# Optimization experiments

Measured on AMD Instinct MI355X. Metric: run time of the kernel, lower is better.

The kernel has to match this reference:

```python
import jax, jax.numpy as jnp
import numpy as np

TEMP = 0.5
EPS = 1e-8  # torch CosineSimilarity eps


def setup_inputs() -> dict:
    key = jax.random.key(0)
    k1, k2 = jax.random.split(key)
    B, D = 4096, 512
    z_i = jax.random.normal(k1, (B, D), dtype=jnp.float32)
    z_j = jax.random.normal(k2, (B, D), dtype=jnp.float32)
    return {"z_i": z_i, "z_j": z_j}


def reference(z_i, z_j):
    B = z_i.shape[0]
    N = 2 * B
    z = jnp.concatenate([z_i, z_j], axis=0)              # [N, D]
    norm = jnp.maximum(jnp.linalg.norm(z, axis=1, keepdims=True), EPS)
    zn = z / norm                                        # unit rows
    sim = jnp.matmul(zn, zn.T) / TEMP                    # [N, N] cosine sims / temperature
    # positives: sim[i, i+B] for i<B and sim[i+B, i] for i<B
    pos = jnp.concatenate([jnp.diagonal(sim, offset=B), jnp.diagonal(sim, offset=-B)])  # [N]
    # CE over logits [pos, negatives] with label 0 == -pos + logsumexp(row without diagonal)
    diag_mask = jnp.eye(N, dtype=bool)
    sim_masked = jnp.where(diag_mask, -jnp.inf, sim)
    lse = jax.nn.logsumexp(sim_masked, axis=1)           # [N]
    loss = jnp.sum(lse - pos) / N                        # CrossEntropyLoss(reduction='sum') / N
    return loss
```

## Files before the change

kernel.cpp:

```cpp
#include <hip/hip_runtime.h>
#include <stdint.h>

#define NROWS 8192
#define HALF_N 4096
#define DIM 512
#define INV_TEMP 2.0f
#define E2SCALE 2.8853900817779268f
#define LN2 0.6931471805599453f
#define NTILES 1056
#define NXCD 8
#define TPX (NTILES / NXCD)

typedef int i32x8 __attribute__((ext_vector_type(8)));
typedef float f32x16 __attribute__((ext_vector_type(16)));

__device__ __forceinline__ void gload_lds16(const unsigned char* g, unsigned char* l) {
  __builtin_amdgcn_global_load_lds(
      (const __attribute__((address_space(1))) unsigned int*)(uintptr_t)g,
      (__attribute__((address_space(3))) unsigned int*)(uint32_t)(uintptr_t)l,
      16, 0, 0);
}

__global__ void __launch_bounds__(256) k_normalize(const float* __restrict__ zi,
                                                   const float* __restrict__ zj,
                                                   unsigned char* __restrict__ zn,
                                                   float* __restrict__ sumexp) {
  int tid = threadIdx.x;
  int gid = blockIdx.x * 256 + tid;
  if (gid < NROWS) sumexp[gid] = 0.0f;
  int wave = tid >> 6, lane = tid & 63;
  int row = blockIdx.x * 4 + wave;
  const float* src = (row < HALF_N) ? (zi + (size_t)row * DIM)
                                    : (zj + (size_t)(row - HALF_N) * DIM);
  const float4* s4 = (const float4*)src;
  float4 a = s4[lane];
  float4 b = s4[lane + 64];
  float ss = a.x * a.x + a.y * a.y + a.z * a.z + a.w * a.w +
             b.x * b.x + b.y * b.y + b.z * b.z + b.w * b.w;
#pragma unroll
  for (int off = 32; off > 0; off >>= 1) ss += __shfl_xor(ss, off, 64);
  float inv = 1.0f / fmaxf(sqrtf(ss), 1e-8f);
  int w0 = __builtin_amdgcn_cvt_pk_fp8_f32(a.x * inv, a.y * inv, 0, false);
  w0 = __builtin_amdgcn_cvt_pk_fp8_f32(a.z * inv, a.w * inv, w0, true);
  int w1 = __builtin_amdgcn_cvt_pk_fp8_f32(b.x * inv, b.y * inv, 0, false);
  w1 = __builtin_amdgcn_cvt_pk_fp8_f32(b.z * inv, b.w * inv, w1, true);
  unsigned char* dst = zn + (size_t)row * DIM;
  *((int*)(dst + lane * 4)) = w0;
  *((int*)(dst + 256 + lane * 4)) = w1;
}

__global__ void __launch_bounds__(256, 2) k_simsum(const unsigned char* __restrict__ zn,
                                                   float* __restrict__ sumexp,
                                                   float* __restrict__ posv) {
  __shared__ __align__(16) unsigned char As[3][256 * 64];
  __shared__ __align__(16) unsigned char Bs[3][128 * 64];
  int tid = threadIdx.x;
  int wave = tid >> 6, lane = tid & 63;

  int b = blockIdx.x;
  int idx = (b & (NXCD - 1)) * TPX + (b >> 3);
  int tm = (int)((65.0f - sqrtf(4225.0f - 4.0f * idx)) * 0.5f);
  while (tm * (65 - tm) > idx) tm--;
  while ((tm + 1) * (64 - tm) <= idx) tm++;
  int tn = idx - tm * (63 - tm);
  int rowBase = tm * 256, colBase = tn * 128;

  int wr = (wave >> 1) * 128, wc = (wave & 1) * 64;
  int h = lane >> 5, c32 = lane & 31;

  int rA = wave * 64 + (lane >> 2);
  int cA = (lane & 3) ^ ((rA >> 1) & 3);
  const unsigned char* gA = zn + (size_t)(rowBase + rA) * DIM + cA * 16;
  int rB = wave * 32 + (lane >> 2);
  int cB = (lane & 3) ^ ((rB >> 1) & 3);
  const unsigned char* gB = zn + (size_t)(colBase + rB) * DIM + cB * 16;

#define STAGE(bf)                                     \
  do {                                                \
    unsigned char* la = &As[bf][wave * 4096];         \
    unsigned char* lb = &Bs[bf][wave * 2048];         \
    gload_lds16(gA, la);                              \
    gload_lds16(gA + 16 * DIM, la + 1024);            \
    gload_lds16(gA + 32 * DIM, la + 2048);            \
    gload_lds16(gA + 48 * DIM, la + 3072);            \
    gload_lds16(gB, lb);                              \
    gload_lds16(gB + 16 * DIM, lb + 1024);            \
    gA += 64; gB += 64;                               \
  } while (0)

  f32x16 acc[4][2];
#pragma unroll
  for (int i = 0; i < 4; i++)
#pragma unroll
    for (int j = 0; j < 2; j++)
#pragma unroll
      for (int r = 0; r < 16; r++) acc[i][j][r] = 0.f;

  int sg = (c32 >> 1) & 3;
  int p0 = (2 * h) ^ sg, p1 = p0 ^ 1;
  int aIdx[4] = {(wr + c32) * 4, (wr + 32 + c32) * 4,
                 (wr + 64 + c32) * 4, (wr + 96 + c32) * 4};
  int bIdx[2] = {(wc + c32) * 4, (wc + 32 + c32) * 4};

#define COMPUTE(bf)                                                                  \
  do {                                                                               \
    const int4* Av = (const int4*)As[bf];                                            \
    const int4* Bv = (const int4*)Bs[bf];                                            \
    i32x8 af[4], bfr[2];                                                             \
    _Pragma("unroll") for (int i = 0; i < 4; i++) {                                  \
      int4 lo = Av[aIdx[i] + p0], hi = Av[aIdx[i] + p1];                             \
      af[i] = (i32x8){lo.x, lo.y, lo.z, lo.w, hi.x, hi.y, hi.z, hi.w};               \
    }                                                                                \
    _Pragma("unroll") for (int j = 0; j < 2; j++) {                                  \
      int4 lo = Bv[bIdx[j] + p0], hi = Bv[bIdx[j] + p1];                             \
      bfr[j] = (i32x8){lo.x, lo.y, lo.z, lo.w, hi.x, hi.y, hi.z, hi.w};              \
    }                                                                                \
    __builtin_amdgcn_s_setprio(1);                                                   \
    _Pragma("unroll") for (int i = 0; i < 4; i++)                                    \
      _Pragma("unroll") for (int j = 0; j < 2; j++)                                  \
        acc[i][j] = __builtin_amdgcn_mfma_scale_f32_32x32x64_f8f6f4(                 \
            af[i], bfr[j], acc[i][j], 0, 0,                               \
            0, 0x7F, 0, 0x7F);                                     \
    __builtin_amdgcn_s_setprio(0);                                                   \
  } while (0)

#define ASM_VMCNT(n) asm volatile("s_waitcnt vmcnt(" #n ")" ::: "memory")
#define WINDOW(s, vm)                                        \
  do {                                                       \
    ASM_VMCNT(vm);                                           \
    asm volatile("s_waitcnt lgkmcnt(0)" ::: "memory");       \
    __builtin_amdgcn_sched_barrier(0);                       \
    __builtin_amdgcn_s_barrier();                            \
    __builtin_amdgcn_sched_barrier(0);                       \
    if ((s) + 2 < 8) STAGE(((s) + 2) % 3);                   \
    COMPUTE((s) % 3);                                        \
  } while (0)

  STAGE(0);
  STAGE(1);
  WINDOW(0, 6);
  WINDOW(1, 6);
  WINDOW(2, 6);
  WINDOW(3, 6);
  WINDOW(4, 6);
  WINDOW(5, 6);
  WINDOW(6, 6);
  WINDOW(7, 0);

  int dbase = colBase + wc - rowBase - wr;
  int rsel = (c32 & 3) | ((c32 >> 3) << 2);
  bool diagLane = (h == ((c32 >> 2) & 1));

#pragma unroll
  for (int i = 0; i < 4; i++)
#pragma unroll
    for (int j = 0; j < 2; j++) {
      int d = dbase + j * 32 - i * 32;
      if (d == HALF_N && diagLane) {
        float sv = acc[i][j][rsel] * INV_TEMP;
        int gr = rowBase + wr + i * 32 + c32;
        posv[gr] = sv;
        posv[gr + HALF_N] = sv;
      }
    }

  float cp[2] = {0.f, 0.f};
#pragma unroll
  for (int i = 0; i < 4; i++) {
    int d0 = dbase - i * 32;
    int d1 = d0 + 32;
#pragma unroll
    for (int r = 0; r < 16; r++) {
      int rowIn = (r & 3) + 8 * (r >> 2) + 4 * h;
      float e0 = __builtin_amdgcn_exp2f(acc[i][0][r] * E2SCALE);
      float e1 = __builtin_amdgcn_exp2f(acc[i][1][r] * E2SCALE);
      bool k0 = (d0 > 0) || ((d0 == 0) && (rowIn < c32));
      bool k1 = (d1 > 0) || ((d1 == 0) && (rowIn < c32));
      e0 = k0 ? e0 : 0.f;
      e1 = k1 ? e1 : 0.f;
      cp[0] += e0;
      cp[1] += e1;
      acc[i][0][r] = e0 + e1;
    }
  }

#define FOLD5(RPX)                                                 \
  do {                                                             \
    _Pragma("unroll") for (int t = 0; t < 16; t++) {               \
      float mine = (lane & 16) ? RPX(t + 16) : RPX(t);             \
      float oth = __shfl_xor((lane & 16) ? RPX(t) : RPX(t + 16), 16, 64); \
      RPX(t) = mine + oth;                                         \
    }                                                              \
    _Pragma("unroll") for (int t = 0; t < 8; t++) {                \
      float mine = (lane & 8) ? RPX(t + 8) : RPX(t);               \
      float oth = __shfl_xor((lane & 8) ? RPX(t) : RPX(t + 8), 8, 64); \
      RPX(t) = mine + oth;                                         \
    }                                                              \
    _Pragma("unroll") for (int t = 0; t < 4; t++) {                \
      float mine = (lane & 4) ? RPX(t + 4) : RPX(t);               \
      float oth = __shfl_xor((lane & 4) ? RPX(t) : RPX(t + 4), 4, 64); \
      RPX(t) = mine + oth;                                         \
    }                                                              \
    _Pragma("unroll") for (int t = 0; t < 2; t++) {                \
      float mine = (lane & 2) ? RPX(t + 2) : RPX(t);               \
      float oth = __shfl_xor((lane & 2) ? RPX(t) : RPX(t + 2), 2, 64); \
      RPX(t) = mine + oth;                                         \
    }                                                              \
    {                                                              \
      float mine = (lane & 1) ? RPX(1) : RPX(0);                   \
      float oth = __shfl_xor((lane & 1) ? RPX(0) : RPX(1), 1, 64); \
      RPX(0) = mine + oth;                                         \
    }                                                              \
  } while (0)

#define RPA(t) acc[(t) >> 4][0][(t) & 15]
#define RPB(t) acc[2 + ((t) >> 4)][0][(t) & 15]
  int myrow = rowBase + wr + 32 * (c32 >> 4) + (c32 & 3) + 8 * ((c32 >> 2) & 3) + 4 * h;
  FOLD5(RPA);
  atomicAdd(&sumexp[myrow], RPA(0));
  FOLD5(RPB);
  atomicAdd(&sumexp[myrow + 64], RPB(0));
#undef RPA
#undef RPB

  cp[0] += __shfl_xor(cp[0], 32, 64);
  cp[1] += __shfl_xor(cp[1], 32, 64);
  float cv = h ? cp[1] : cp[0];
  atomicAdd(&sumexp[colBase + wc + h * 32 + c32], cv);
#undef STAGE
#undef COMPUTE
#undef WINDOW
#undef ASM_VMCNT
#undef FOLD5
}

__global__ void __launch_bounds__(1024) k_final(const float* __restrict__ sumexp,
                                                const float* __restrict__ posv,
                                                float* __restrict__ out) {
  __shared__ float red[16];
  int tid = threadIdx.x;
  const float4* se4 = (const float4*)sumexp;
  const float4* pv4 = (const float4*)posv;
  float p = 0.f;
#pragma unroll
  for (int c = 0; c < 2; c++) {
    float4 se = se4[tid * 2 + c];
    float4 pv = pv4[tid * 2 + c];
    p += (__builtin_amdgcn_logf(se.x) + __builtin_amdgcn_logf(se.y) +
          __builtin_amdgcn_logf(se.z) + __builtin_amdgcn_logf(se.w)) * LN2 -
         (pv.x + pv.y + pv.z + pv.w);
  }
#pragma unroll
  for (int off = 32; off > 0; off >>= 1) p += __shfl_xor(p, off, 64);
  int wv = tid >> 6, ln = tid & 63;
  if (ln == 0) red[wv] = p;
  __syncthreads();
  if (tid == 0) {
    float t = 0.f;
    for (int w = 0; w < 16; w++) t += red[w];
    out[0] = t / (float)NROWS;
  }
}

extern "C" void kernel_launch(void* const* d_in, const int* in_sizes, int n_in,
                              void* d_out, int out_size, void* d_ws, size_t ws_size,
                              hipStream_t stream) {
  const float* zi = (const float*)d_in[0];
  const float* zj = (const float*)d_in[1];
  unsigned char* zn = (unsigned char*)d_ws;
  float* sumexp = (float*)((char*)d_ws + (size_t)NROWS * DIM);
  float* posv = sumexp + NROWS;
  float* out = (float*)d_out;

  hipLaunchKernelGGL(k_normalize, dim3(2048), dim3(256), 0, stream, zi, zj, zn, sumexp);
  hipLaunchKernelGGL(k_simsum, dim3(NTILES), dim3(256), 0, stream, zn, sumexp, posv);
  hipLaunchKernelGGL(k_final, dim3(1), dim3(1024), 0, stream, sumexp, posv, out);
}
```

Measured before the change: 97.15 us.

## Load MFMA operands directly from global memory into registers, dropping LDS staging

Replaces the triple-buffered LDS pipeline (global_load_lds plus barriers) with per-wave direct global loads of the fp8 operand fragments into registers, double-buffered across K steps. This removes LDS traffic, s_barrier synchronisation and LDS occupancy limits. In exchange, operand rows shared between waves are now fetched redundantly from global/L2, and many more VGPRs are needed for the two register buffers, which may hurt occupancy or latency hiding.

```diff
diff --git a/kernel.cpp b/kernel.cpp
--- a/kernel.cpp
+++ b/kernel.cpp
@@ -13,13 +13,6 @@
 
 typedef int i32x8 __attribute__((ext_vector_type(8)));
 typedef float f32x16 __attribute__((ext_vector_type(16)));
-
-__device__ __forceinline__ void gload_lds16(const unsigned char* g, unsigned char* l) {
-  __builtin_amdgcn_global_load_lds(
-      (const __attribute__((address_space(1))) unsigned int*)(uintptr_t)g,
-      (__attribute__((address_space(3))) unsigned int*)(uint32_t)(uintptr_t)l,
-      16, 0, 0);
-}
 
 __global__ void __launch_bounds__(256) k_normalize(const float* __restrict__ zi,
                                                    const float* __restrict__ zj,
@@ -52,8 +45,6 @@
 __global__ void __launch_bounds__(256, 2) k_simsum(const unsigned char* __restrict__ zn,
                                                    float* __restrict__ sumexp,
                                                    float* __restrict__ posv) {
-  __shared__ __align__(16) unsigned char As[3][256 * 64];
-  __shared__ __align__(16) unsigned char Bs[3][128 * 64];
   int tid = threadIdx.x;
   int wave = tid >> 6, lane = tid & 63;
 
@@ -68,84 +59,78 @@
   int wr = (wave >> 1) * 128, wc = (wave & 1) * 64;
   int h = lane >> 5, c32 = lane & 31;
 
-  int rA = wave * 64 + (lane >> 2);
-  int cA = (lane & 3) ^ ((rA >> 1) & 3);
-  const unsigned char* gA = zn + (size_t)(rowBase + rA) * DIM + cA * 16;
-  int rB = wave * 32 + (lane >> 2);
-  int cB = (lane & 3) ^ ((rB >> 1) & 3);
-  const unsigned char* gB = zn + (size_t)(colBase + rB) * DIM + cB * 16;
-
-#define STAGE(bf)                                     \
-  do {                                                \
-    unsigned char* la = &As[bf][wave * 4096];         \
-    unsigned char* lb = &Bs[bf][wave * 2048];         \
-    gload_lds16(gA, la);                              \
-    gload_lds16(gA + 16 * DIM, la + 1024);            \
-    gload_lds16(gA + 32 * DIM, la + 2048);            \
-    gload_lds16(gA + 48 * DIM, la + 3072);            \
-    gload_lds16(gB, lb);                              \
-    gload_lds16(gB + 16 * DIM, lb + 1024);            \
-    gA += 64; gB += 64;                               \
+  const unsigned char* pA0 = zn + (size_t)(rowBase + wr + c32) * DIM + h * 32;
+  const unsigned char* pA1 = pA0 + 32 * DIM;
+  const unsigned char* pA2 = pA0 + 64 * DIM;
+  const unsigned char* pA3 = pA0 + 96 * DIM;
+  const unsigned char* pB0 = zn + (size_t)(colBase + wc + c32) * DIM + h * 32;
+  const unsigned char* pB1 = pB0 + 32 * DIM;
+
+  f32x16 acc[4][2];
+#pragma unroll
+  for (int i = 0; i < 4; i++)
+#pragma unroll
+    for (int j = 0; j < 2; j++)
+#pragma unroll
+      for (int r = 0; r < 16; r++) acc[i][j][r] = 0.f;
+
+#define PACK8(lo, hi) ((i32x8){lo.x, lo.y, lo.z, lo.w, hi.x, hi.y, hi.z, hi.w})
+#define MF(a, b, c)                                                       \
+  __builtin_amdgcn_mfma_scale_f32_32x32x64_f8f6f4((a), (b), (c), 0, 0,    \
+                                                  0, 0x7F, 0, 0x7F)
+
+  int4 Xa0l, Xa0h, Xa1l, Xa1h, Xa2l, Xa2h, Xa3l, Xa3h, Xb0l, Xb0h, Xb1l, Xb1h;
+  int4 Ya0l, Ya0h, Ya1l, Ya1h, Ya2l, Ya2h, Ya3l, Ya3h, Yb0l, Yb0h, Yb1l, Yb1h;
+
+#define LOADSET(P, koff)                                                  \
+  do {                                                                    \
+    P##a0l = *(const int4*)(pA0 + (koff));                                \
+    P##a0h = *(const int4*)(pA0 + (koff) + 16);                           \
+    P##a1l = *(const int4*)(pA1 + (koff));                                \
+    P##a1h = *(const int4*)(pA1 + (koff) + 16);                           \
+    P##a2l = *(const int4*)(pA2 + (koff));                                \
+    P##a2h = *(const int4*)(pA2 + (koff) + 16);                           \
+    P##a3l = *(const int4*)(pA3 + (koff));                                \
+    P##a3h = *(const int4*)(pA3 + (koff) + 16);                           \
+    P##b0l = *(const int4*)(pB0 + (koff));                                \
+    P##b0h = *(const int4*)(pB0 + (koff) + 16);                           \
+    P##b1l = *(const int4*)(pB1 + (koff));                                \
+    P##b1h = *(const int4*)(pB1 + (koff) + 16);                           \
   } while (0)
 
-  f32x16 acc[4][2];
-#pragma unroll
-  for (int i = 0; i < 4; i++)
-#pragma unroll
-    for (int j = 0; j < 2; j++)
-#pragma unroll
-      for (int r = 0; r < 16; r++) acc[i][j][r] = 0.f;
-
-  int sg = (c32 >> 1) & 3;
-  int p0 = (2 * h) ^ sg, p1 = p0 ^ 1;
-  int aIdx[4] = {(wr + c32) * 4, (wr + 32 + c32) * 4,
-                 (wr + 64 + c32) * 4, (wr + 96 + c32) * 4};
-  int bIdx[2] = {(wc + c32) * 4, (wc + 32 + c32) * 4};
-
-#define COMPUTE(bf)                                                                  \
-  do {                                                                               \
-    const int4* Av = (const int4*)As[bf];                                            \
-    const int4* Bv = (const int4*)Bs[bf];                                            \
-    i32x8 af[4], bfr[2];                                                             \
-    _Pragma("unroll") for (int i = 0; i < 4; i++) {                                  \
-      int4 lo = Av[aIdx[i] + p0], hi = Av[aIdx[i] + p1];                             \
-      af[i] = (i32x8){lo.x, lo.y, lo.z, lo.w, hi.x, hi.y, hi.z, hi.w};               \
-    }                                                                                \
-    _Pragma("unroll") for (int j = 0; j < 2; j++) {                                  \
-      int4 lo = Bv[bIdx[j] + p0], hi = Bv[bIdx[j] + p1];                             \
-      bfr[j] = (i32x8){lo.x, lo.y, lo.z, lo.w, hi.x, hi.y, hi.z, hi.w};              \
-    }                                                                                \
-    __builtin_amdgcn_s_setprio(1);                                                   \
-    _Pragma("unroll") for (int i = 0; i < 4; i++)                                    \
-      _Pragma("unroll") for (int j = 0; j < 2; j++)                                  \
-        acc[i][j] = __builtin_amdgcn_mfma_scale_f32_32x32x64_f8f6f4(                 \
-            af[i], bfr[j], acc[i][j], 0, 0,                               \
-            0, 0x7F, 0, 0x7F);                                     \
-    __builtin_amdgcn_s_setprio(0);                                                   \
+#define MFMASET(P)                                                        \
+  do {                                                                    \
+    i32x8 af0 = PACK8(P##a0l, P##a0h), af1 = PACK8(P##a1l, P##a1h);       \
+    i32x8 af2 = PACK8(P##a2l, P##a2h), af3 = PACK8(P##a3l, P##a3h);       \
+    i32x8 bf0 = PACK8(P##b0l, P##b0h), bf1 = PACK8(P##b1l, P##b1h);      \
+    __builtin_amdgcn_s_setprio(1);                                        \
+    acc[0][0] = MF(af0, bf0, acc[0][0]);                                  \
+    acc[0][1] = MF(af0, bf1, acc[0][1]);                                  \
+    acc[1][0] = MF(af1, bf0, acc[1][0]);                                  \
+    acc[1][1] = MF(af1, bf1, acc[1][1]);                                  \
+    acc[2][0] = MF(af2, bf0, acc[2][0]);                                  \
+    acc[2][1] = MF(af2, bf1, acc[2][1]);                                  \
+    acc[3][0] = MF(af3, bf0, acc[3][0]);                                  \
+    acc[3][1] = MF(af3, bf1, acc[3][1]);                                  \
+    __builtin_amdgcn_s_setprio(0);                                        \
   } while (0)
 
-#define ASM_VMCNT(n) asm volatile("s_waitcnt vmcnt(" #n ")" ::: "memory")
-#define WINDOW(s, vm)                                        \
-  do {                                                       \
-    ASM_VMCNT(vm);                                           \
-    asm volatile("s_waitcnt lgkmcnt(0)" ::: "memory");       \
-    __builtin_amdgcn_sched_barrier(0);                       \
-    __builtin_amdgcn_s_barrier();                            \
-    __builtin_amdgcn_sched_barrier(0);                       \
-    if ((s) + 2 < 8) STAGE(((s) + 2) % 3);                   \
-    COMPUTE((s) % 3);                                        \
-  } while (0)
-
-  STAGE(0);
-  STAGE(1);
-  WINDOW(0, 6);
-  WINDOW(1, 6);
-  WINDOW(2, 6);
-  WINDOW(3, 6);
-  WINDOW(4, 6);
-  WINDOW(5, 6);
-  WINDOW(6, 6);
-  WINDOW(7, 0);
+  LOADSET(X, 0);
+  LOADSET(Y, 64);
+  MFMASET(X);
+  LOADSET(X, 128);
+  MFMASET(Y);
+  LOADSET(Y, 192);
+  MFMASET(X);
+  LOADSET(X, 256);
+  MFMASET(Y);
+  LOADSET(Y, 320);
+  MFMASET(X);
+  LOADSET(X, 384);
+  MFMASET(Y);
+  LOADSET(Y, 448);
+  MFMASET(X);
+  MFMASET(Y);
 
   int dbase = colBase + wc - rowBase - wr;
   int rsel = (c32 & 3) | ((c32 >> 3) << 2);
@@ -227,10 +212,10 @@
   cp[1] += __shfl_xor(cp[1], 32, 64);
   float cv = h ? cp[1] : cp[0];
   atomicAdd(&sumexp[colBase + wc + h * 32 + c32], cv);
-#undef STAGE
-#undef COMPUTE
-#undef WINDOW
-#undef ASM_VMCNT
+#undef PACK8
+#undef MF
+#undef LOADSET
+#undef MFMASET
 #undef FOLD5
 }
 
```

New measurement: 157.3 us. 62.0% more time.
